# Optimization experiments

Measured on AMD Instinct MI355X. Metric: run time of the kernel, lower is better.

The kernel has to match this reference:

```python
import jax, jax.numpy as jnp
import numpy as np

TEMPERATURE = 0.2


def setup_inputs() -> dict:
    key = jax.random.key(0)
    k1, k2, k3, k4 = jax.random.split(key, 4)
    B, D, K, C = 8192, 128, 10, 10
    x = jax.random.normal(k1, (B, D), dtype=jnp.float32)
    x_aug = jax.random.normal(k2, (B, D), dtype=jnp.float32)
    hard_q = jax.random.randint(k3, (2, B), 0, C, dtype=jnp.int64)
    neg_q = jax.random.randint(k4, (2, B, K), 0, C, dtype=jnp.int64)
    return {"x": x, "x_aug": x_aug, "hard_q": hard_q, "neg_q": neg_q,
            "num_clusters": C}


def reference(x, x_aug, hard_q, neg_q, num_clusters):
    B = x.shape[0]
    N = 2 * B
    # L2-normalize both views and concatenate: out is [2B, D]
    out_1 = x / jnp.linalg.norm(x, axis=1, keepdims=True)
    out_2 = x_aug / jnp.linalg.norm(x_aug, axis=1, keepdims=True)
    out = jnp.concatenate([out_1, out_2], axis=0)

    hq = hard_q.reshape(N)            # [2B] cluster id per sample
    nq = neg_q.reshape(N, -1)         # [2B, K] negative cluster ids per row

    # exp(similarity / T): [2B, 2B]
    sim_matrix = jnp.exp(jnp.matmul(out, out.T) / TEMPERATURE)

    # membership[i, j] = (hard_q[j] in neg_q[i]).
    # Build a small [2B, C] cluster-membership table instead of a [2B,2B,K]
    # broadcast to keep memory low, then gather columns by hq.
    cluster_ids = jnp.arange(num_clusters)                       # [C]
    table = jnp.any(nq[:, :, None] == cluster_ids[None, None, :], axis=1)  # [2B, C]
    member = table[:, hq]                                        # [2B, 2B]

    eye = jnp.eye(N, dtype=bool)
    mask = member & ~eye

    # Original code does masked_select (flatten) then .sum(dim=-1), which
    # reduces over ALL selected entries -> a single scalar denominator.
    denom = jnp.sum(jnp.where(mask, sim_matrix, jnp.float32(0.0)))

    pos = jnp.exp(jnp.sum(out_1 * out_2, axis=-1) / TEMPERATURE)  # [B]
    pos = jnp.concatenate([pos, pos], axis=0)                     # [2B]

    loss = jnp.mean(-jnp.log(pos / denom))
    return loss
```

## Files before the change

kernel.cpp:

```cpp
#include <hip/hip_runtime.h>
#include <hip/hip_bf16.h>

typedef __attribute__((ext_vector_type(8))) __bf16 bf16x8;
typedef __attribute__((ext_vector_type(4))) float f32x4;

#define SCALE 2.68588886f

static __device__ __forceinline__ float fastexp2(float x) {
#if __has_builtin(__builtin_amdgcn_exp2f)
    return __builtin_amdgcn_exp2f(x);
#else
    return exp2f(x);
#endif
}


__global__ __launch_bounds__(256) void normalize_kernel(
    const float* __restrict__ x, const float* __restrict__ xa,
    __bf16* __restrict__ outb, float* __restrict__ pos_parts, int B)
{
    __shared__ float sdot[4];
    int wave = threadIdx.x >> 6;
    int lane = threadIdx.x & 63;
    int row = blockIdx.x * 4 + wave;
    const float2* px = (const float2*)(x  + (size_t)row * 128);
    const float2* pa = (const float2*)(xa + (size_t)row * 128);
    float2 v1 = px[lane];
    float2 v2 = pa[lane];
    float s1 = v1.x * v1.x + v1.y * v1.y;
    float s2 = v2.x * v2.x + v2.y * v2.y;
    float d  = v1.x * v2.x + v1.y * v2.y;
    #pragma unroll
    for (int off = 32; off; off >>= 1) {
        s1 += __shfl_xor(s1, off);
        s2 += __shfl_xor(s2, off);
        d  += __shfl_xor(d,  off);
    }
    float rn1 = rsqrtf(s1) * SCALE;
    float rn2 = rsqrtf(s2) * SCALE;
    __bf16* o1 = outb + (size_t)row * 128;
    __bf16* o2 = outb + (size_t)(B + row) * 128;
    o1[2 * lane]     = (__bf16)(v1.x * rn1);
    o1[2 * lane + 1] = (__bf16)(v1.y * rn1);
    o2[2 * lane]     = (__bf16)(v2.x * rn2);
    o2[2 * lane + 1] = (__bf16)(v2.y * rn2);
    if (lane == 0) sdot[wave] = d * rsqrtf(s1) * rsqrtf(s2);
    __syncthreads();
    if (threadIdx.x == 0)
        pos_parts[blockIdx.x] = sdot[0] + sdot[1] + sdot[2] + sdot[3];
}

__global__ __launch_bounds__(256, 4) void sim_kernel(
    const __bf16* __restrict__ outb, const int* __restrict__ hq,
    const int* __restrict__ nq, float* __restrict__ denom_parts)
{
    int wgid = (blockIdx.x & 7) * 1032 + (blockIdx.x >> 3);

    int rem = wgid;
    int I = 0;
    #pragma unroll 1
    while (true) {
        int rc = 136 + (7 - I) * 256;
        if (rem < rc) break;
        rem -= rc; ++I;
    }
    int bi, bj;
    if (rem < 136) {
        int ti = 0;
        #pragma unroll 1
        while (rem >= 16 - ti) { rem -= 16 - ti; ++ti; }
        bi = I * 16 + ti;
        bj = I * 16 + ti + rem;
    } else {
        rem -= 136;
        int J = I + 1 + (rem >> 8);
        int local = rem & 255;
        bi = I * 16 + (local >> 4);
        bj = J * 16 + (local & 15);
    }

    __shared__ float4 sbuf[2][2][512];
    __shared__ unsigned sMU[128];
    __shared__ unsigned sMV[128];
    __shared__ float red[4];

    int tid = threadIdx.x;

    const float4* gA = (const float4*)(outb + (size_t)bi * 128 * 128);
    const float4* gB = (const float4*)(outb + (size_t)bj * 128 * 128);

    int r0 = tid >> 2, c0 = tid & 3;
    int g0 = r0 * 16 + c0;
    int g1 = g0 + 64 * 16;
    int s0 = r0 * 4 + (c0 ^ ((r0 >> 1) & 3));
    int s1 = s0 + 64 * 4;

    float4 la0 = gA[g0], la1 = gA[g1];
    float4 lb0 = gB[g0], lb1 = gB[g1];

    {
        int half = tid >> 7;
        int idx = tid & 127;
        int row = (half ? bj : bi) * 128 + idx;
        const int* p = nq + (size_t)row * 10;
        unsigned b = 0;
        #pragma unroll
        for (int k = 0; k < 10; ++k) b |= 1u << (p[k] & 31);
        unsigned h = (unsigned)hq[row];
        if (half) sMV[idx] = (1u << h) | (b << 10);
        else      sMU[idx] = b | (1u << (10 + h));
    }

    sbuf[0][0][s0] = la0; sbuf[0][0][s1] = la1;
    sbuf[0][1][s0] = lb0; sbuf[0][1][s1] = lb1;
    __syncthreads();

    int wave = tid >> 6, lane = tid & 63;
    int wr = (wave >> 1) * 64;
    int wc = (wave & 1) * 64;
    int lrow = lane & 15, quad = lane >> 4;

    f32x4 acc[4][4] = {};

    #pragma unroll
    for (int p = 0; p < 4; ++p) {
        int pb = p & 1;
        if (p < 3) {
            la0 = gA[g0 + (p + 1) * 4]; la1 = gA[g1 + (p + 1) * 4];
            lb0 = gB[g0 + (p + 1) * 4]; lb1 = gB[g1 + (p + 1) * 4];
        }
        const __bf16* Ab = (const __bf16*)sbuf[pb][0];
        const __bf16* Bb = (const __bf16*)sbuf[pb][1];
        bf16x8 a[4], b[4];
        #pragma unroll
        for (int m = 0; m < 4; ++m) {
            int r = wr + m * 16 + lrow;
            a[m] = *(const bf16x8*)&Ab[r * 32 + ((quad ^ ((r >> 1) & 3)) << 3)];
        }
        #pragma unroll
        for (int n = 0; n < 4; ++n) {
            int r = wc + n * 16 + lrow;
            b[n] = *(const bf16x8*)&Bb[r * 32 + ((quad ^ ((r >> 1) & 3)) << 3)];
        }
        __builtin_amdgcn_s_setprio(1);
        #pragma unroll
        for (int m = 0; m < 4; ++m)
            #pragma unroll
            for (int n = 0; n < 4; ++n)
                acc[m][n] = __builtin_amdgcn_mfma_f32_16x16x32_bf16(
                    a[m], b[n], acc[m][n], 0, 0, 0);
        __builtin_amdgcn_s_setprio(0);
        if (p < 3) {
            sbuf[pb ^ 1][0][s0] = la0; sbuf[pb ^ 1][0][s1] = la1;
            sbuf[pb ^ 1][1][s0] = lb0; sbuf[pb ^ 1][1][s1] = lb1;
            __syncthreads();
        }
    }

    unsigned mv[4], mu[4][4];
    #pragma unroll
    for (int n = 0; n < 4; ++n) mv[n] = sMV[wc + n * 16 + lrow];
    #pragma unroll
    for (int m = 0; m < 4; ++m)
        #pragma unroll
        for (int r = 0; r < 4; ++r) mu[m][r] = sMU[wr + m * 16 + quad * 4 + r];

    float ls[4] = {0.0f, 0.0f, 0.0f, 0.0f};
    #pragma unroll
    for (int m = 0; m < 4; ++m) {
        #pragma unroll
        for (int n = 0; n < 4; ++n) {
            #pragma unroll
            for (int r = 0; r < 4; ++r) {
                float w = (float)__popc(mu[m][r] & mv[n]);
                ls[r] += fastexp2(acc[m][n][r]) * w;
            }
        }
    }
    float lsum = (ls[0] + ls[1]) + (ls[2] + ls[3]);

    bool diag = (bi == bj);
    if (diag && (wr == wc) && ((lrow >> 2) == quad)) {
        int rd = lrow & 3;
        float sub = 0.0f;
        #pragma unroll
        for (int m = 0; m < 4; ++m) {
            float wd = (float)__popc(mu[m][rd] & mv[m]);
            sub += fastexp2(acc[m][m][rd]) * wd;
        }
        lsum -= sub;
    }
    if (diag) lsum *= 0.5f;

    #pragma unroll
    for (int off = 32; off; off >>= 1) lsum += __shfl_down(lsum, off);
    if (lane == 0) red[wave] = lsum;
    __syncthreads();
    if (tid == 0)
        denom_parts[blockIdx.x] = red[0] + red[1] + red[2] + red[3];
}

__global__ __launch_bounds__(1024) void finalize_kernel(
    const float* __restrict__ denom_parts, const float* __restrict__ pos_parts,
    float* __restrict__ out, float invB, int nd, int np)
{
    __shared__ float sred[32];
    int tid = threadIdx.x;
    float d = 0.0f, p = 0.0f;
    for (int i = tid; i < nd; i += 1024) d += denom_parts[i];
    for (int i = tid; i < np; i += 1024) p += pos_parts[i];
    #pragma unroll
    for (int off = 32; off; off >>= 1) {
        d += __shfl_down(d, off);
        p += __shfl_down(p, off);
    }
    int wv = tid >> 6, ln = tid & 63;
    if (ln == 0) { sred[wv] = d; sred[16 + wv] = p; }
    __syncthreads();
    if (tid == 0) {
        float D = 0.0f, P = 0.0f;
        #pragma unroll
        for (int i = 0; i < 16; ++i) { D += sred[i]; P += sred[16 + i]; }
        out[0] = logf(D) - 5.0f * P * invB;
    }
}

extern "C" void kernel_launch(void* const* d_in, const int* in_sizes, int n_in,
                              void* d_out, int out_size, void* d_ws, size_t ws_size,
                              hipStream_t stream) {
    const float* x  = (const float*)d_in[0];
    const float* xa = (const float*)d_in[1];
    const int* hq   = (const int*)d_in[2];
    const int* nq   = (const int*)d_in[3];
    int B = in_sizes[0] / 128;
    int N = 2 * B;
    int T = N / 128;
    int nblocks = T * (T + 1) / 2;

    char* ws = (char*)d_ws;
    float* denom_parts = (float*)ws;
    float* pos_parts   = (float*)(ws + 33024);
    __bf16* outb       = (__bf16*)(ws + 41216);

    normalize_kernel<<<B / 4, 256, 0, stream>>>(x, xa, outb, pos_parts, B);
    sim_kernel<<<nblocks, 256, 0, stream>>>(outb, hq, nq, denom_parts);
    finalize_kernel<<<1, 1024, 0, stream>>>(denom_parts, pos_parts,
                                            (float*)d_out, 1.0f / (float)B,
                                            nblocks, B / 4);
}
```

Baseline: 127.1 us.

## Use 512-thread workgroups with 64x32 wave tiles in sim kernel

Doubles the sim kernel's workgroup to 8 waves. Each wave now computes a 64x32 sub-tile instead of 64x64, and each thread loads one float4 per operand per stage instead of two. This cuts accumulator registers per wave and aims for higher occupancy and more latency hiding. The diagonal-exclusion correction is folded into per-element weights in the main exp loop instead of a separate subtraction pass. In exchange, each wave re-reads more A fragments from LDS relative to its MFMA work.

After: 245.2 us. +92.9%, slower.

```diff
diff --git a/kernel.cpp b/kernel.cpp
--- a/kernel.cpp
+++ b/kernel.cpp
@@ -50,7 +50,7 @@
         pos_parts[blockIdx.x] = sdot[0] + sdot[1] + sdot[2] + sdot[3];
 }
 
-__global__ __launch_bounds__(256, 4) void sim_kernel(
+__global__ __launch_bounds__(512, 8) void sim_kernel(
     const __bf16* __restrict__ outb, const int* __restrict__ hq,
     const int* __restrict__ nq, float* __restrict__ denom_parts)
 {
@@ -82,7 +82,7 @@
     __shared__ float4 sbuf[2][2][512];
     __shared__ unsigned sMU[128];
     __shared__ unsigned sMV[128];
-    __shared__ float red[4];
+    __shared__ float red[8];
 
     int tid = threadIdx.x;
 
@@ -91,14 +91,12 @@
 
     int r0 = tid >> 2, c0 = tid & 3;
     int g0 = r0 * 16 + c0;
-    int g1 = g0 + 64 * 16;
     int s0 = r0 * 4 + (c0 ^ ((r0 >> 1) & 3));
-    int s1 = s0 + 64 * 4;
-
-    float4 la0 = gA[g0], la1 = gA[g1];
-    float4 lb0 = gB[g0], lb1 = gB[g1];
-
-    {
+
+    float4 la = gA[g0];
+    float4 lb = gB[g0];
+
+    if (tid < 256) {
         int half = tid >> 7;
         int idx = tid & 127;
         int row = (half ? bj : bi) * 128 + idx;
@@ -111,34 +109,34 @@
         else      sMU[idx] = b | (1u << (10 + h));
     }
 
-    sbuf[0][0][s0] = la0; sbuf[0][0][s1] = la1;
-    sbuf[0][1][s0] = lb0; sbuf[0][1][s1] = lb1;
+    sbuf[0][0][s0] = la;
+    sbuf[0][1][s0] = lb;
     __syncthreads();
 
     int wave = tid >> 6, lane = tid & 63;
-    int wr = (wave >> 1) * 64;
-    int wc = (wave & 1) * 64;
+    int wr = (wave >> 2) * 64;
+    int wc = (wave & 3) * 32;
     int lrow = lane & 15, quad = lane >> 4;
 
-    f32x4 acc[4][4] = {};
+    f32x4 acc[4][2] = {};
 
     #pragma unroll
     for (int p = 0; p < 4; ++p) {
         int pb = p & 1;
         if (p < 3) {
-            la0 = gA[g0 + (p + 1) * 4]; la1 = gA[g1 + (p + 1) * 4];
-            lb0 = gB[g0 + (p + 1) * 4]; lb1 = gB[g1 + (p + 1) * 4];
+            la = gA[g0 + (p + 1) * 4];
+            lb = gB[g0 + (p + 1) * 4];
         }
         const __bf16* Ab = (const __bf16*)sbuf[pb][0];
         const __bf16* Bb = (const __bf16*)sbuf[pb][1];
-        bf16x8 a[4], b[4];
+        bf16x8 a[4], b[2];
         #pragma unroll
         for (int m = 0; m < 4; ++m) {
             int r = wr + m * 16 + lrow;
             a[m] = *(const bf16x8*)&Ab[r * 32 + ((quad ^ ((r >> 1) & 3)) << 3)];
         }
         #pragma unroll
-        for (int n = 0; n < 4; ++n) {
+        for (int n = 0; n < 2; ++n) {
             int r = wc + n * 16 + lrow;
             b[n] = *(const bf16x8*)&Bb[r * 32 + ((quad ^ ((r >> 1) & 3)) << 3)];
         }
@@ -146,58 +144,65 @@
         #pragma unroll
         for (int m = 0; m < 4; ++m)
             #pragma unroll
-            for (int n = 0; n < 4; ++n)
+            for (int n = 0; n < 2; ++n)
                 acc[m][n] = __builtin_amdgcn_mfma_f32_16x16x32_bf16(
                     a[m], b[n], acc[m][n], 0, 0, 0);
         __builtin_amdgcn_s_setprio(0);
         if (p < 3) {
-            sbuf[pb ^ 1][0][s0] = la0; sbuf[pb ^ 1][0][s1] = la1;
-            sbuf[pb ^ 1][1][s0] = lb0; sbuf[pb ^ 1][1][s1] = lb1;
+            sbuf[pb ^ 1][0][s0] = la;
+            sbuf[pb ^ 1][1][s0] = lb;
             __syncthreads();
         }
     }
 
-    unsigned mv[4], mu[4][4];
-    #pragma unroll
-    for (int n = 0; n < 4; ++n) mv[n] = sMV[wc + n * 16 + lrow];
+    unsigned mv[2], mu[4][4];
+    #pragma unroll
+    for (int n = 0; n < 2; ++n) mv[n] = sMV[wc + n * 16 + lrow];
     #pragma unroll
     for (int m = 0; m < 4; ++m)
         #pragma unroll
         for (int r = 0; r < 4; ++r) mu[m][r] = sMU[wr + m * 16 + quad * 4 + r];
 
+    bool diag = (bi == bj);
+    int dOff = wc - wr;
+    bool waveDiag = diag && (dOff == 0 || dOff == 32);
+    bool lane_diag = waveDiag && ((lrow >> 2) == quad);
+    bool m_eq_n = (dOff == 0);
+    int rd = lrow & 3;
+    float wk0[4], wk2[4];
+    #pragma unroll
+    for (int r = 0; r < 4; ++r) {
+        wk0[r] = (lane_diag &&  m_eq_n && r == rd) ? 0.0f : 1.0f;
+        wk2[r] = (lane_diag && !m_eq_n && r == rd) ? 0.0f : 1.0f;
+    }
+
     float ls[4] = {0.0f, 0.0f, 0.0f, 0.0f};
     #pragma unroll
     for (int m = 0; m < 4; ++m) {
         #pragma unroll
-        for (int n = 0; n < 4; ++n) {
+        for (int n = 0; n < 2; ++n) {
             #pragma unroll
             for (int r = 0; r < 4; ++r) {
                 float w = (float)__popc(mu[m][r] & mv[n]);
+                if (m == n)     w *= wk0[r];
+                if (m == n + 2) w *= wk2[r];
                 ls[r] += fastexp2(acc[m][n][r]) * w;
             }
         }
     }
     float lsum = (ls[0] + ls[1]) + (ls[2] + ls[3]);
-
-    bool diag = (bi == bj);
-    if (diag && (wr == wc) && ((lrow >> 2) == quad)) {
-        int rd = lrow & 3;
-        float sub = 0.0f;
-        #pragma unroll
-        for (int m = 0; m < 4; ++m) {
-            float wd = (float)__popc(mu[m][rd] & mv[m]);
-            sub += fastexp2(acc[m][m][rd]) * wd;
-        }
-        lsum -= sub;
-    }
     if (diag) lsum *= 0.5f;
 
     #pragma unroll
     for (int off = 32; off; off >>= 1) lsum += __shfl_down(lsum, off);
     if (lane == 0) red[wave] = lsum;
     __syncthreads();
-    if (tid == 0)
-        denom_parts[blockIdx.x] = red[0] + red[1] + red[2] + red[3];
+    if (tid == 0) {
+        float s = 0.0f;
+        #pragma unroll
+        for (int i = 0; i < 8; ++i) s += red[i];
+        denom_parts[blockIdx.x] = s;
+    }
 }
 
 __global__ __launch_bounds__(1024) void finalize_kernel(
@@ -243,7 +248,7 @@
     __bf16* outb       = (__bf16*)(ws + 41216);
 
     normalize_kernel<<<B / 4, 256, 0, stream>>>(x, xa, outb, pos_parts, B);
-    sim_kernel<<<nblocks, 256, 0, stream>>>(outb, hq, nq, denom_parts);
+    sim_kernel<<<nblocks, 512, 0, stream>>>(outb, hq, nq, denom_parts);
     finalize_kernel<<<1, 1024, 0, stream>>>(denom_parts, pos_parts,
                                             (float*)d_out, 1.0f / (float)B,
                                             nblocks, B / 4);
```
